# Performance work log

Hardware: AMD Instinct MI355X
Metric: run time of the kernel (lower is better)

The kernel has to match this reference:

```python
import jax, jax.numpy as jnp
import numpy as np

B, N = 2, 131072          # batch, expanded node slots (divisible by flag_size)
FEAT = 69                 # org(3) + pos(3) + uids(63)
KERNELS = 128
FLAG_SIZE = 4             # 1 << dims, dims = 2
BINS = 16                 # 1 << flag_size


def _conv1d(x, w, b, stride=1, padding='SAME'):
    # keras Conv1D: x [B,N,Cin], w [K,Cin,Cout], relu activation
    y = jax.lax.conv_general_dilated(x, w, (stride,), padding,
                                     dimension_numbers=('NWC', 'WIO', 'NWC'))
    return jax.nn.relu(y + b)


def setup_inputs() -> dict:
    key = jax.random.key(0)
    ks = jax.random.split(key, 12)

    def g(k, shape):
        fan_in = int(np.prod(shape[:-1]))
        return (jax.random.normal(k, shape, jnp.float32) / np.sqrt(fan_in)).astype(jnp.float32)

    c_x = FEAT + KERNELS                 # 197 after each pre conv concat
    c_flags = 2 * FEAT + KERNELS         # 266 flags-head input
    c_sym = c_flags + FLAG_SIZE          # 270 symbols-branch input

    return {
        'inputs': jax.random.normal(ks[0], (B, N, FEAT), jnp.float32),
        'w_pre0': g(ks[1], (3, FEAT, KERNELS)),   'b_pre0': jnp.zeros((KERNELS,), jnp.float32),
        'w_pre1': g(ks[2], (3, c_x, KERNELS)),    'b_pre1': jnp.zeros((KERNELS,), jnp.float32),
        'w_flags': g(ks[3], (c_flags, FLAG_SIZE)), 'b_flags': jnp.zeros((FLAG_SIZE,), jnp.float32),
        'w_merge': g(ks[4], (FLAG_SIZE, c_sym, KERNELS)), 'b_merge': jnp.zeros((KERNELS,), jnp.float32),
        'w_post0': g(ks[5], (3, KERNELS, KERNELS)), 'b_post0': jnp.zeros((KERNELS,), jnp.float32),
        'w_post1': g(ks[6], (3, KERNELS, KERNELS)), 'b_post1': jnp.zeros((KERNELS,), jnp.float32),
        'w_post2': g(ks[7], (3, KERNELS, KERNELS)), 'b_post2': jnp.zeros((KERNELS,), jnp.float32),
        'w_post3': g(ks[8], (3, KERNELS, KERNELS)), 'b_post3': jnp.zeros((KERNELS,), jnp.float32),
        'w_sym': g(ks[9], (KERNELS, BINS)),        'b_sym': jnp.zeros((BINS,), jnp.float32),
    }


def _forward(inputs, w_pre0, b_pre0, w_pre1, b_pre1, w_flags, b_flags,
             w_merge, b_merge, w_post0, b_post0, w_post1, b_post1,
             w_post2, b_post2, w_post3, b_post3, w_sym, b_sym):
    # pos offsets = (3, 6); pos = inputs[..., 3:5] (2 columns)
    pos = inputs[..., 3:5]
    sort = jnp.argsort(pos, axis=-2)                       # [B, N, 2]
    # gather with batch_dims=1 along node axis
    X = jnp.take_along_axis(inputs, sort[..., 1:2], axis=1)   # sorted by pos col 1
    x0 = jax.lax.stop_gradient(X)                            # [B, N, 69]
    X = jnp.concatenate([x0, _conv1d(X, w_pre0, b_pre0)], axis=-1)  # [B, N, 197]
    X = jnp.concatenate([x0, _conv1d(X, w_pre1, b_pre1)], axis=-1)  # [B, N, 197]
    X = jnp.concatenate([X, jnp.take_along_axis(inputs, sort[..., 0:1], axis=1)], axis=-1)  # [B, N, 266]

    F = jax.nn.sigmoid(X @ w_flags + b_flags)               # [B, N, 4]

    S = jax.lax.stop_gradient(jnp.concatenate([F, X], axis=-1))     # [B, N, 270]
    S = _conv1d(S, w_merge, b_merge, stride=FLAG_SIZE, padding='VALID')  # [B, N/4, 128]
    for w, b in ((w_post0, b_post0), (w_post1, b_post1), (w_post2, b_post2), (w_post3, b_post3)):
        S = _conv1d(S, w, b)
    S = jax.nn.softmax(S @ w_sym + b_sym, axis=-1)          # [B, N/4, 16]

    Fd = (F[..., 0] - F[..., 1]).reshape(F.shape[0], -1, FLAG_SIZE)  # [B, N/4, 4]
    return jnp.concatenate([Fd, S], axis=-1)                # [B, N/4, 20]


def reference(inputs, w_pre0, b_pre0, w_pre1, b_pre1, w_flags, b_flags,
              w_merge, b_merge, w_post0, b_post0, w_post1, b_post1,
              w_post2, b_post2, w_post3, b_post3, w_sym, b_sym):
    return _forward(inputs, w_pre0, b_pre0, w_pre1, b_pre1, w_flags, b_flags,
                    w_merge, b_merge, w_post0, b_post0, w_post1, b_post1,
                    w_post2, b_post2, w_post3, b_post3, w_sym, b_sym)
```

## Files before the change

### kernel.cpp

```cpp
#include <hip/hip_runtime.h>
#include <hip/hip_bf16.h>
#include <math.h>

#define NPOS 131072
#define NF   69
#define NMRG 32768
#define TILE 2048
#define TPS  64
#define NSORT 4
#define EPT  16
#define XCW  288

typedef __attribute__((ext_vector_type(8))) short short8;
typedef __attribute__((ext_vector_type(4))) short s16x4;
typedef __bf16 bf16x8 __attribute__((ext_vector_type(8)));
typedef __attribute__((ext_vector_type(4))) float f32x4;

static __device__ inline bf16x8 as_bf16x8(short8 v){ union{short8 s; bf16x8 b;} u; u.s=v; return u.b; }
static __device__ inline short f2bf(float x){ __hip_bfloat16 h = __float2bfloat16(x); return *(short*)&h; }
static __device__ inline float bf2f(short s){ return __uint_as_float(((unsigned)(unsigned short)s)<<16); }

static __device__ inline void gld16(const short* g, short* l){
  __builtin_amdgcn_global_load_lds(
      (const __attribute__((address_space(1))) unsigned int*)g,
      (__attribute__((address_space(3))) unsigned int*)l, 16, 0, 0);
}

__global__ void k_make_keys(const float* __restrict__ inp, unsigned* __restrict__ kA,
                            unsigned* __restrict__ vA){
  unsigned t = blockIdx.x*256u + threadIdx.x;
  unsigned s = t >> 17, i = t & (NPOS-1u);
  unsigned b = s >> 1, ch = 3u + (s & 1u);
  float x = inp[((size_t)b*NPOS + i)*NF + ch];
  unsigned u = __float_as_uint(x);
  u = (u & 0x80000000u) ? ~u : (u | 0x80000000u);
  kA[t] = u; vA[t] = i;
}

__global__ __launch_bounds__(256) void k_hist(const unsigned* __restrict__ src,
                                              unsigned* __restrict__ hist, int shift){
  __shared__ unsigned h[256];
  int tid = threadIdx.x;
  h[tid] = 0u; __syncthreads();
  int s = blockIdx.x / TPS, tile = blockIdx.x % TPS;
  const unsigned* ks = src + (size_t)s*NPOS + (size_t)tile*TILE;
  for (int r = 0; r < TILE/256; ++r){
    unsigned d = (ks[r*256 + tid] >> shift) & 255u;
    atomicAdd(&h[d], 1u);
  }
  __syncthreads();
  hist[s*16384 + tid*TPS + tile] = h[tid];
}

__global__ __launch_bounds__(256) void k_scan(unsigned* __restrict__ hist){
  __shared__ unsigned tot[256];
  int tid = threadIdx.x; int s = blockIdx.x;
  unsigned* g = hist + s*16384;
  unsigned sum = 0;
  for (int q = 0; q < TPS; ++q) sum += g[tid*TPS + q];
  tot[tid] = sum;
  __syncthreads();
  if (tid == 0){
    unsigned run = 0;
    for (int t = 0; t < 256; ++t){ unsigned tmp = tot[t]; tot[t] = run; run += tmp; }
  }
  __syncthreads();
  unsigned run = tot[tid];
  for (int q = 0; q < TPS; ++q){ unsigned tmp = g[tid*TPS+q]; g[tid*TPS+q] = run; run += tmp; }
}

__global__ __launch_bounds__(128) void k_scatter(const unsigned* __restrict__ srcK,
    const unsigned* __restrict__ srcV, unsigned* __restrict__ dstK, unsigned* __restrict__ dstV,
    const unsigned* __restrict__ off, int shift){
  __shared__ unsigned short cnt[256*128];
  int tid = threadIdx.x;
  unsigned* cz = (unsigned*)cnt;
  for (int idx = tid; idx < 256*128/2; idx += 128) cz[idx] = 0u;
  __syncthreads();
  int s = blockIdx.x / TPS, tile = blockIdx.x % TPS;
  const unsigned* ks = srcK + (size_t)s*NPOS + (size_t)tile*TILE;
  const unsigned* vs = srcV + (size_t)s*NPOS + (size_t)tile*TILE;
  unsigned k8[EPT], v8[EPT];
  #pragma unroll
  for (int r = 0; r < EPT; ++r){
    k8[r] = ks[tid*EPT + r];
    v8[r] = vs[tid*EPT + r];
    unsigned d = (k8[r] >> shift) & 255u;
    cnt[d*128 + tid]++;
  }
  __syncthreads();
  for (int dd = 0; dd < 2; ++dd){
    int d = tid + dd*128;
    unsigned run = 0;
    for (int t = 0; t < 128; ++t){ unsigned tmp = cnt[d*128 + t]; cnt[d*128 + t] = (unsigned short)run; run += tmp; }
  }
  __syncthreads();
  const unsigned* ob = off + s*16384;
  #pragma unroll
  for (int r = 0; r < EPT; ++r){
    unsigned d = (k8[r] >> shift) & 255u;
    unsigned rk = cnt[d*128 + tid];
    cnt[d*128 + tid] = (unsigned short)(rk + 1u);
    unsigned pos = ob[d*TPS + tile] + rk;
    dstK[(size_t)s*NPOS + pos] = k8[r];
    dstV[(size_t)s*NPOS + pos] = v8[r];
  }
}

__global__ __launch_bounds__(256) void k_cvt(const float* __restrict__ inp,
                                             short* __restrict__ inpb, int b){
  int t = blockIdx.x*256 + threadIdx.x;
  int i = t/9, q = t - i*9;
  const float* sp = inp + ((size_t)b*NPOS + i)*NF + q*8;
  short o[8];
  #pragma unroll
  for (int e = 0; e < 8; ++e){
    int c = q*8 + e;
    o[e] = (c < NF) ? f2bf(sp[e]) : (short)0;
  }
  *(short8*)(inpb + (size_t)i*72 + q*8) = *(short8*)o;
}

__global__ __launch_bounds__(256) void k_gath2(const short* __restrict__ inpb,
    const unsigned* __restrict__ P1, const unsigned* __restrict__ P0,
    short* __restrict__ XA, short* __restrict__ Xcat){
  int t = blockIdx.x*256 + threadIdx.x;
  int i = t/18, u = t - i*18;
  int p = u/9, q = u - p*9;
  if (p){
    short8 v = *(const short8*)(inpb + (size_t)P1[i]*72 + q*8);
    *(short8*)(XA + (size_t)i*224 + 128 + q*8) = v;
    s16x4 lo = {v[0],v[1],v[2],v[3]}, hi = {v[4],v[5],v[6],v[7]};
    *(s16x4*)(Xcat + (size_t)i*XCW + 132 + q*8) = lo;
    *(s16x4*)(Xcat + (size_t)i*XCW + 136 + q*8) = hi;
  } else {
    short8 v = *(const short8*)(inpb + (size_t)P0[i]*72 + q*8);
    *(short8*)(Xcat + (size_t)i*XCW + 208 + q*8) = v;
    if (q == 8){
      s16x4 z4 = {0,0,0,0};
      *(s16x4*)(Xcat + (size_t)i*XCW + 204) = z4;
      short8 z8 = {0,0,0,0,0,0,0,0};
      *(short8*)(Xcat + (size_t)i*XCW + 280) = z8;
    }
  }
}

__global__ void k_prepB(const float* __restrict__ w, short* __restrict__ out,
                        int KC, int NQ, int mode, int total){
  int t = blockIdx.x*256 + threadIdx.x;
  if (t >= total) return;
  int lane = t & 63, ni = (t>>6) & 1, ksub = (t>>7) & 1;
  int rest = t >> 8;
  int q = rest % NQ;
  int wv = rest / NQ;
  int tap = q / KC, cc = q - tap*KC;
  int nn = wv*32 + ni*16 + (lane & 15);
  int chb = cc*64 + ksub*32 + ((lane >> 4) & 3)*8;
  short o[8];
  #pragma unroll
  for (int e = 0; e < 8; ++e){
    int ch = chb + e;
    float val = 0.f;
    if (mode == 0){ if (ch < 69)  val = w[((size_t)tap*69  + ch)*128 + nn]; }
    else if (mode == 1){
      if (ch < 128)      val = w[((size_t)tap*197 + 69 + ch)*128 + nn];
      else if (ch < 197) val = w[((size_t)tap*197 + ch - 128)*128 + nn];
    }
    else if (mode == 2){ if (ch < 128) val = w[((size_t)tap*128 + ch)*128 + nn]; }
    else {
      int tm = ch / XCW, cm = ch - tm*XCW;
      int orig = -1;
      if (cm < 128)                     orig = 73 + cm;
      else if (cm < 201)                orig = cm - 128;
      else if (cm >= 208 && cm < 277)   orig = cm - 7;
      if (orig >= 0) val = w[((size_t)tm*270 + orig)*128 + nn];
    }
    o[e] = f2bf(val);
  }
  *(short8*)(out + (size_t)t*8) = *(short8*)o;
}

__global__ void k_prepWf(const float* __restrict__ wf, float* __restrict__ out){
  int t = blockIdx.x*256 + threadIdx.x;
  if (t >= XCW*4) return;
  int c = t >> 2, q = t & 3;
  float v = 0.f;
  if (c < 128)                  v = wf[(69 + c)*4 + q];
  else if (c >= 132 && c < 201) v = wf[(c - 132)*4 + q];
  else if (c >= 208 && c < 277) v = wf[(197 + c - 208)*4 + q];
  out[t] = v;
}

#define OSTR 132

template<int CPAD>
__global__ __launch_bounds__(256) void k_conv3p(
    const short* __restrict__ src, int sstride, int coff, int cin,
    const short* __restrict__ wB, const float* __restrict__ bias,
    short* __restrict__ dst, int dstride, int n)
{
  constexpr int KC = CPAD/64;
  constexpr int NSTEP2 = 3*KC*2;
  constexpr int PF = 4;
  constexpr int ASTR = CPAD + 8;
  constexpr int AG = CPAD/8;
  constexpr size_t ABYTES = (size_t)66*ASTR*2;
  constexpr size_t OBYTES = (size_t)64*OSTR*4;
  constexpr size_t LBYTES = (ABYTES > OBYTES) ? ABYTES : OBYTES;
  __shared__ __attribute__((aligned(16))) char LDS[LBYTES];
  short* A_s = (short*)LDS;
  float* OT  = (float*)LDS;
  int tid = threadIdx.x;
  int i0 = blockIdx.x*64;
  int wv = tid >> 6, lane = tid & 63;
  int lm = lane & 15, lk = lane >> 4;

  const short* wBw = wB + (size_t)wv*NSTEP2*1024 + (size_t)lane*8;
  auto LB = [&](int ss, int ni){
    return as_bf16x8(*(const short8*)(wBw + (ss*2 + ni)*512));
  };
  bf16x8 bq[PF][2];
  #pragma unroll
  for (int s = 0; s < PF; ++s){ bq[s][0] = LB(s,0); bq[s][1] = LB(s,1); }

  for (int idx = tid; idx < 66*AG; idx += 256){
    int r = idx / AG, g = idx - r*AG;
    int pos = i0 - 1 + r;
    short8 v = {0,0,0,0,0,0,0,0};
    if (pos >= 0 && pos < n && g*8 < cin){
      const short* sp = src + (size_t)pos*sstride + coff + g*8;
      if (g*8 + 8 <= cin) v = *(const short8*)sp;
      else { for (int j = 0; g*8 + j < cin; ++j) v[j] = sp[j]; }
    }
    *(short8*)(A_s + r*ASTR + g*8) = v;
  }
  __syncthreads();

  f32x4 acc[4][2] = {};
  #pragma unroll
  for (int ss = 0; ss < NSTEP2; ++ss){
    int slot = ss % PF;
    bf16x8 b0 = bq[slot][0], b1 = bq[slot][1];
    if (ss + PF < NSTEP2){ bq[slot][0] = LB(ss+PF,0); bq[slot][1] = LB(ss+PF,1); }
    int q = ss >> 1, ksub = ss & 1;
    int tp = q / KC, c = q - tp*KC;
    bf16x8 a[4];
    #pragma unroll
    for (int mi = 0; mi < 4; ++mi)
      a[mi] = as_bf16x8(*(const short8*)(A_s + (mi*16+lm+tp)*ASTR + c*64 + ksub*32 + lk*8));
    #pragma unroll
    for (int mi = 0; mi < 4; ++mi){
      acc[mi][0] = __builtin_amdgcn_mfma_f32_16x16x32_bf16(a[mi], b0, acc[mi][0], 0, 0, 0);
      acc[mi][1] = __builtin_amdgcn_mfma_f32_16x16x32_bf16(a[mi], b1, acc[mi][1], 0, 0, 0);
    }
  }
  __syncthreads();
  float b0s = bias[wv*32 + lm], b1s = bias[wv*32 + 16 + lm];
  #pragma unroll
  for (int mi = 0; mi < 4; ++mi)
    #pragma unroll
    for (int ni = 0; ni < 2; ++ni){
      float bb = ni ? b1s : b0s;
      #pragma unroll
      for (int r = 0; r < 4; ++r)
        OT[(mi*16 + lk*4 + r)*OSTR + wv*32 + ni*16 + lm] = fmaxf(acc[mi][ni][r] + bb, 0.f);
    }
  __syncthreads();
  {
    int r = tid >> 2, q = tid & 3;
    const float* row = OT + r*OSTR + q*32;
    short o[32];
    #pragma unroll
    for (int jc = 0; jc < 8; ++jc){
      f32x4 v = *(const f32x4*)(row + jc*4);
      #pragma unroll
      for (int e = 0; e < 4; ++e) o[jc*4+e] = f2bf(v[e]);
    }
    short* dp = dst + (size_t)(i0 + r)*dstride + q*32;
    #pragma unroll
    for (int v8 = 0; v8 < 4; ++v8) *(short8*)(dp + v8*8) = *(short8*)(o + v8*8);
  }
}

__global__ __launch_bounds__(256) void k_mergem3(const short* __restrict__ Xf,
    const short* __restrict__ wB, const float* __restrict__ bias, short* __restrict__ dst)
{
  constexpr int NS = 4*XCW/64;
  constexpr size_t OBYTES = (size_t)64*OSTR*4;
  __shared__ __attribute__((aligned(16))) char LDS[OBYTES];
  short* A_s = (short*)LDS;
  float* OT  = (float*)LDS;
  int tid = threadIdx.x;
  int j0 = blockIdx.x*64;
  int wv = tid >> 6, lane = tid & 63;
  int lm = lane & 15, lk = lane >> 4;
  auto stageA = [&](int s){
    #pragma unroll
    for (int it = 0; it < 2; ++it){
      int slot = it*256 + tid;
      int r = slot >> 3, kv = slot & 7;
      const short* gp = Xf + (size_t)(j0 + r)*(4*XCW) + s*64 + ((kv ^ (r&7))*8);
      gld16(gp, A_s + (s&1)*4096 + slot*8);
    }
  };
  const short* wBl = wB + (size_t)wv*NS*2048 + (size_t)lane*8;
  auto LB = [&](int s, int ks, int ni){
    return as_bf16x8(*(const short8*)(wBl + ((size_t)(s*2 + ks)*2 + ni)*512));
  };
  bf16x8 c00 = LB(0,0,0), c01 = LB(0,0,1), c10 = LB(0,1,0), c11 = LB(0,1,1);
  stageA(0);
  __syncthreads();
  f32x4 acc[4][2] = {};
  for (int s = 0; s < NS; ++s){
    bf16x8 n00, n01, n10, n11;
    if (s < NS-1){
      n00 = LB(s+1,0,0); n01 = LB(s+1,0,1); n10 = LB(s+1,1,0); n11 = LB(s+1,1,1);
      stageA(s+1);
    }
    const short* Ab = A_s + (s&1)*4096;
    bf16x8 a[4];
    #pragma unroll
    for (int mi = 0; mi < 4; ++mi){
      int r = mi*16 + lm;
      a[mi] = as_bf16x8(*(const short8*)(Ab + r*64 + ((lk ^ (r&7))*8)));
    }
    #pragma unroll
    for (int mi = 0; mi < 4; ++mi){
      acc[mi][0] = __builtin_amdgcn_mfma_f32_16x16x32_bf16(a[mi], c00, acc[mi][0], 0, 0, 0);
      acc[mi][1] = __builtin_amdgcn_mfma_f32_16x16x32_bf16(a[mi], c01, acc[mi][1], 0, 0, 0);
    }
    #pragma unroll
    for (int mi = 0; mi < 4; ++mi){
      int r = mi*16 + lm;
      a[mi] = as_bf16x8(*(const short8*)(Ab + r*64 + (((4+lk) ^ (r&7))*8)));
    }
    #pragma unroll
    for (int mi = 0; mi < 4; ++mi){
      acc[mi][0] = __builtin_amdgcn_mfma_f32_16x16x32_bf16(a[mi], c10, acc[mi][0], 0, 0, 0);
      acc[mi][1] = __builtin_amdgcn_mfma_f32_16x16x32_bf16(a[mi], c11, acc[mi][1], 0, 0, 0);
    }
    __syncthreads();
    c00 = n00; c01 = n01; c10 = n10; c11 = n11;
  }
  float b0 = bias[wv*32 + lm], b1 = bias[wv*32 + 16 + lm];
  #pragma unroll
  for (int mi = 0; mi < 4; ++mi)
    #pragma unroll
    for (int ni = 0; ni < 2; ++ni){
      float bb = ni ? b1 : b0;
      #pragma unroll
      for (int r = 0; r < 4; ++r)
        OT[(mi*16 + lk*4 + r)*OSTR + wv*32 + ni*16 + lm] = fmaxf(acc[mi][ni][r] + bb, 0.f);
    }
  __syncthreads();
  {
    int r = tid >> 2, q = tid & 3;
    const float* row = OT + r*OSTR + q*32;
    short o[32];
    #pragma unroll
    for (int jc = 0; jc < 8; ++jc){
      f32x4 v = *(const f32x4*)(row + jc*4);
      #pragma unroll
      for (int e = 0; e < 4; ++e) o[jc*4+e] = f2bf(v[e]);
    }
    short* dp = dst + (size_t)(j0 + r)*128 + q*32;
    #pragma unroll
    for (int v8 = 0; v8 < 4; ++v8) *(short8*)(dp + v8*8) = *(short8*)(o + v8*8);
  }
}

__global__ __launch_bounds__(256) void k_flags2(short* __restrict__ Xcat,
    const float* __restrict__ Wf2, const float* __restrict__ bf, float* __restrict__ F){
  size_t i = (size_t)blockIdx.x*256 + threadIdx.x;
  const short* x = Xcat + i*XCW;
  float a0 = bf[0], a1 = bf[1], a2 = bf[2], a3 = bf[3];
  for (int g = 0; g < XCW/8; ++g){
    short8 x8 = *(const short8*)(x + g*8);
    #pragma unroll
    for (int e = 0; e < 8; ++e){
      float xv = bf2f(x8[e]);
      const float* w = Wf2 + (g*8+e)*4;
      a0 = fmaf(xv,w[0],a0); a1 = fmaf(xv,w[1],a1); a2 = fmaf(xv,w[2],a2); a3 = fmaf(xv,w[3],a3);
    }
  }
  float f0 = 1.f/(1.f+expf(-a0)), f1 = 1.f/(1.f+expf(-a1));
  float f2 = 1.f/(1.f+expf(-a2)), f3 = 1.f/(1.f+expf(-a3));
  float* f = F + i*4;
  f[0]=f0; f[1]=f1; f[2]=f2; f[3]=f3;
  short* xc = Xcat + i*XCW + 128;
  xc[0]=f2bf(f0); xc[1]=f2bf(f1); xc[2]=f2bf(f2); xc[3]=f2bf(f3);
}

__global__ __launch_bounds__(256) void k_out(const short* __restrict__ S,
    const float* __restrict__ F, const float* __restrict__ Ws, const float* __restrict__ bs,
    float* __restrict__ out, int b){
  size_t j = (size_t)blockIdx.x*256 + threadIdx.x;
  float l[16];
  #pragma unroll
  for (int t = 0; t < 16; ++t) l[t] = bs[t];
  const short* s = S + j*128;
  for (int g = 0; g < 16; ++g){
    short8 x8 = *(const short8*)(s + g*8);
    #pragma unroll
    for (int e = 0; e < 8; ++e){
      float x = bf2f(x8[e]);
      const float* w = Ws + (g*8+e)*16;
      #pragma unroll
      for (int t = 0; t < 16; ++t) l[t] = fmaf(x, w[t], l[t]);
    }
  }
  float m = l[0];
  #pragma unroll
  for (int t = 1; t < 16; ++t) m = fmaxf(m, l[t]);
  float sum = 0.f;
  #pragma unroll
  for (int t = 0; t < 16; ++t){ l[t] = expf(l[t]-m); sum += l[t]; }
  float inv = 1.f/sum;
  float* o = out + ((size_t)b*NMRG + j)*20;
  #pragma unroll
  for (int k = 0; k < 4; ++k){
    size_t r = (size_t)(4*j + k)*4;
    o[k] = F[r] - F[r+1];
  }
  #pragma unroll
  for (int t = 0; t < 16; ++t) o[4+t] = l[t]*inv;
}

extern "C" void kernel_launch(void* const* d_in, const int* in_sizes, int n_in,
                              void* d_out, int out_size, void* d_ws, size_t ws_size,
                              hipStream_t stream){
  const float* inp     = (const float*)d_in[0];
  const float* w_pre0  = (const float*)d_in[1];
  const float* b_pre0  = (const float*)d_in[2];
  const float* w_pre1  = (const float*)d_in[3];
  const float* b_pre1  = (const float*)d_in[4];
  const float* w_flags = (const float*)d_in[5];
  const float* b_flags = (const float*)d_in[6];
  const float* w_merge = (const float*)d_in[7];
  const float* b_merge = (const float*)d_in[8];
  const float* w_post[4] = {(const float*)d_in[9], (const float*)d_in[11],
                            (const float*)d_in[13], (const float*)d_in[15]};
  const float* b_post[4] = {(const float*)d_in[10], (const float*)d_in[12],
                            (const float*)d_in[14], (const float*)d_in[16]};
  const float* w_sym   = (const float*)d_in[17];
  const float* b_sym   = (const float*)d_in[18];
  float* outp = (float*)d_out;

  char* p = (char*)d_ws;
  unsigned* kA = (unsigned*)p; p += (size_t)NSORT*NPOS*4;
  unsigned* vA = (unsigned*)p; p += (size_t)NSORT*NPOS*4;
  unsigned* kB = (unsigned*)p; p += (size_t)NSORT*NPOS*4;
  unsigned* vB = (unsigned*)p; p += (size_t)NSORT*NPOS*4;
  unsigned* hist = (unsigned*)p; p += (size_t)NSORT*16384*4;
  short* inpb = (short*)p; p += (size_t)NPOS*72*2;
  short* XA   = (short*)p; p += (size_t)NPOS*224*2;
  short* Xcat = (short*)p; p += (size_t)NPOS*XCW*2;
  float* Fbuf = (float*)p; p += (size_t)NPOS*4*4;
  short* M0   = (short*)p; p += (size_t)NMRG*128*2;
  short* M1   = (short*)p; p += (size_t)NMRG*128*2;
  short* wb0  = (short*)p; p += (size_t)3*2*8192*2;
  short* wb1  = (short*)p; p += (size_t)3*4*8192*2;
  short* wbq0 = (short*)p; p += (size_t)3*2*8192*2;
  short* wbq1 = (short*)p; p += (size_t)3*2*8192*2;
  short* wbq2 = (short*)p; p += (size_t)3*2*8192*2;
  short* wbq3 = (short*)p; p += (size_t)3*2*8192*2;
  short* wbm  = (short*)p; p += (size_t)18*8192*2;
  float* wf2  = (float*)p; p += (size_t)XCW*4*4;
  if ((size_t)(p - (char*)d_ws) > ws_size) return;
  short* wbq[4] = {wbq0, wbq1, wbq2, wbq3};

  k_prepB<<<(6144 +255)/256, 256, 0, stream>>>(w_pre0, wb0, 2, 6, 0, 6144);
  k_prepB<<<(12288+255)/256, 256, 0, stream>>>(w_pre1, wb1, 4, 12, 1, 12288);
  for (int i = 0; i < 4; ++i)
    k_prepB<<<(6144+255)/256, 256, 0, stream>>>(w_post[i], wbq[i], 2, 6, 2, 6144);
  k_prepB<<<(18432+255)/256, 256, 0, stream>>>(w_merge, wbm, 18, 18, 3, 18432);
  k_prepWf<<<(XCW*4+255)/256, 256, 0, stream>>>(w_flags, wf2);

  k_make_keys<<<NSORT*NPOS/256, 256, 0, stream>>>(inp, kA, vA);
  unsigned *sk = kA, *sv = vA, *dk = kB, *dv = vB;
  for (int pass = 0; pass < 4; ++pass){
    int shift = pass*8;
    k_hist<<<NSORT*TPS, 256, 0, stream>>>(sk, hist, shift);
    k_scan<<<NSORT, 256, 0, stream>>>(hist);
    k_scatter<<<NSORT*TPS, 128, 0, stream>>>(sk, sv, dk, dv, hist, shift);
    unsigned* t;
    t = sk; sk = dk; dk = t;
    t = sv; sv = dv; dv = t;
  }
  for (int b = 0; b < 2; ++b){
    const unsigned* P0 = sv + (size_t)(b*2+0)*NPOS;
    const unsigned* P1 = sv + (size_t)(b*2+1)*NPOS;
    k_cvt<<<NPOS*9/256, 256, 0, stream>>>(inp, inpb, b);
    k_gath2<<<NPOS*18/256, 256, 0, stream>>>(inpb, P1, P0, XA, Xcat);
    k_conv3p<128><<<NPOS/64, 256, 0, stream>>>(XA, 224, 128, 69,  wb0, b_pre0, XA,   224, NPOS);
    k_conv3p<256><<<NPOS/64, 256, 0, stream>>>(XA, 224, 0,   197, wb1, b_pre1, Xcat, XCW, NPOS);
    k_flags2<<<NPOS/256, 256, 0, stream>>>(Xcat, wf2, b_flags, Fbuf);
    k_mergem3<<<NMRG/64, 256, 0, stream>>>(Xcat, wbm, b_merge, M0);
    k_conv3p<128><<<NMRG/64, 256, 0, stream>>>(M0, 128, 0, 128, wbq[0], b_post[0], M1, 128, NMRG);
    k_conv3p<128><<<NMRG/64, 256, 0, stream>>>(M1, 128, 0, 128, wbq[1], b_post[1], M0, 128, NMRG);
    k_conv3p<128><<<NMRG/64, 256, 0, stream>>>(M0, 128, 0, 128, wbq[2], b_post[2], M1, 128, NMRG);
    k_conv3p<128><<<NMRG/64, 256, 0, stream>>>(M1, 128, 0, 128, wbq[3], b_post[3], M0, 128, NMRG);
    k_out<<<NMRG/256, 256, 0, stream>>>(M0, Fbuf, w_sym, b_sym, outp, b);
  }
}
```

Baseline: 598.8 us.

## Split conv input channels into halves, shrink tiles, stage bf16 output in LDS

```diff
diff --git a/kernel.cpp b/kernel.cpp
--- a/kernel.cpp
+++ b/kernel.cpp
@@ -191,65 +191,83 @@
   out[t] = v;
 }
 
-#define OSTR 132
-
-template<int CPAD>
-__global__ __launch_bounds__(256) void k_conv3p(
+#define OSTR2 136
+
+template<int CPAD, int MT>
+__global__ __launch_bounds__(256) void k_conv3s(
     const short* __restrict__ src, int sstride, int coff, int cin,
     const short* __restrict__ wB, const float* __restrict__ bias,
     short* __restrict__ dst, int dstride, int n)
 {
-  constexpr int KC = CPAD/64;
-  constexpr int NSTEP2 = 3*KC*2;
-  constexpr int PF = 4;
-  constexpr int ASTR = CPAD + 8;
-  constexpr int AG = CPAD/8;
-  constexpr size_t ABYTES = (size_t)66*ASTR*2;
-  constexpr size_t OBYTES = (size_t)64*OSTR*4;
+  constexpr int KC  = CPAD/64;
+  constexpr int KH  = CPAD/2;
+  constexpr int KC2 = KH/64;
+  constexpr int SPH = 3*KC2*2;
+  constexpr int NST = 2*SPH;
+  constexpr int PF  = 4;
+  constexpr int ASTR = KH + 8;
+  constexpr int AG  = KH/8;
+  constexpr int MI  = MT/16;
+  constexpr size_t ABYTES = (size_t)(MT+2)*ASTR*2;
+  constexpr size_t OBYTES = (size_t)MT*OSTR2*2;
   constexpr size_t LBYTES = (ABYTES > OBYTES) ? ABYTES : OBYTES;
   __shared__ __attribute__((aligned(16))) char LDS[LBYTES];
   short* A_s = (short*)LDS;
-  float* OT  = (float*)LDS;
+  short* OTs = (short*)LDS;
   int tid = threadIdx.x;
-  int i0 = blockIdx.x*64;
+  int i0 = blockIdx.x*MT;
   int wv = tid >> 6, lane = tid & 63;
   int lm = lane & 15, lk = lane >> 4;
 
-  const short* wBw = wB + (size_t)wv*NSTEP2*1024 + (size_t)lane*8;
-  auto LB = [&](int ss, int ni){
-    return as_bf16x8(*(const short8*)(wBw + (ss*2 + ni)*512));
+  const short* wBw = wB + (size_t)wv*(KC*6)*1024 + (size_t)lane*8;
+  auto LB = [&](int ls, int ni){
+    int h = ls / SPH, r1 = ls % SPH;
+    int tp = r1 / (KC2*2), r2 = r1 % (KC2*2);
+    int c = r2 >> 1, ksub = r2 & 1;
+    int q = tp*KC + h*KC2 + c;
+    return as_bf16x8(*(const short8*)(wBw + ((q*2 + ksub)*2 + ni)*512));
   };
+  auto stageA = [&](int h){
+    for (int idx = tid; idx < (MT+2)*AG; idx += 256){
+      int r = idx / AG, g = idx - r*AG;
+      int pos = i0 - 1 + r;
+      int cb = h*KH + g*8;
+      short8 v = {0,0,0,0,0,0,0,0};
+      if (pos >= 0 && pos < n && cb < cin){
+        const short* sp = src + (size_t)pos*sstride + coff + cb;
+        if (cb + 8 <= cin) v = *(const short8*)sp;
+        else { for (int j = 0; cb + j < cin; ++j) v[j] = sp[j]; }
+      }
+      *(short8*)(A_s + r*ASTR + g*8) = v;
+    }
+  };
+
   bf16x8 bq[PF][2];
   #pragma unroll
   for (int s = 0; s < PF; ++s){ bq[s][0] = LB(s,0); bq[s][1] = LB(s,1); }
-
-  for (int idx = tid; idx < 66*AG; idx += 256){
-    int r = idx / AG, g = idx - r*AG;
-    int pos = i0 - 1 + r;
-    short8 v = {0,0,0,0,0,0,0,0};
-    if (pos >= 0 && pos < n && g*8 < cin){
-      const short* sp = src + (size_t)pos*sstride + coff + g*8;
-      if (g*8 + 8 <= cin) v = *(const short8*)sp;
-      else { for (int j = 0; g*8 + j < cin; ++j) v[j] = sp[j]; }
-    }
-    *(short8*)(A_s + r*ASTR + g*8) = v;
-  }
-  __syncthreads();
-
-  f32x4 acc[4][2] = {};
-  #pragma unroll
-  for (int ss = 0; ss < NSTEP2; ++ss){
-    int slot = ss % PF;
+  stageA(0);
+  __syncthreads();
+
+  f32x4 acc[MI][2] = {};
+  #pragma unroll
+  for (int ls = 0; ls < NST; ++ls){
+    if (ls == SPH){
+      __syncthreads();
+      stageA(1);
+      __syncthreads();
+    }
+    int slot = ls % PF;
     bf16x8 b0 = bq[slot][0], b1 = bq[slot][1];
-    if (ss + PF < NSTEP2){ bq[slot][0] = LB(ss+PF,0); bq[slot][1] = LB(ss+PF,1); }
-    int q = ss >> 1, ksub = ss & 1;
-    int tp = q / KC, c = q - tp*KC;
-    bf16x8 a[4];
-    #pragma unroll
-    for (int mi = 0; mi < 4; ++mi)
+    if (ls + PF < NST){ bq[slot][0] = LB(ls+PF,0); bq[slot][1] = LB(ls+PF,1); }
+    int r1 = ls % SPH;
+    int tp = r1 / (KC2*2), r2 = r1 % (KC2*2);
+    int c = r2 >> 1, ksub = r2 & 1;
+    bf16x8 a[MI];
+    #pragma unroll
+    for (int mi = 0; mi < MI; ++mi)
       a[mi] = as_bf16x8(*(const short8*)(A_s + (mi*16+lm+tp)*ASTR + c*64 + ksub*32 + lk*8));
     #pragma unroll
-    for (int mi = 0; mi < 4; ++mi){
+    for (int mi = 0; mi < MI; ++mi){
       acc[mi][0] = __builtin_amdgcn_mfma_f32_16x16x32_bf16(a[mi], b0, acc[mi][0], 0, 0, 0);
       acc[mi][1] = __builtin_amdgcn_mfma_f32_16x16x32_bf16(a[mi], b1, acc[mi][1], 0, 0, 0);
     }
@@ -257,51 +275,45 @@
   __syncthreads();
   float b0s = bias[wv*32 + lm], b1s = bias[wv*32 + 16 + lm];
   #pragma unroll
-  for (int mi = 0; mi < 4; ++mi)
+  for (int mi = 0; mi < MI; ++mi)
     #pragma unroll
     for (int ni = 0; ni < 2; ++ni){
       float bb = ni ? b1s : b0s;
       #pragma unroll
       for (int r = 0; r < 4; ++r)
-        OT[(mi*16 + lk*4 + r)*OSTR + wv*32 + ni*16 + lm] = fmaxf(acc[mi][ni][r] + bb, 0.f);
+        OTs[(mi*16 + lk*4 + r)*OSTR2 + wv*32 + ni*16 + lm] = f2bf(fmaxf(acc[mi][ni][r] + bb, 0.f));
     }
   __syncthreads();
   {
-    int r = tid >> 2, q = tid & 3;
-    const float* row = OT + r*OSTR + q*32;
-    short o[32];
-    #pragma unroll
-    for (int jc = 0; jc < 8; ++jc){
-      f32x4 v = *(const f32x4*)(row + jc*4);
-      #pragma unroll
-      for (int e = 0; e < 4; ++e) o[jc*4+e] = f2bf(v[e]);
-    }
-    short* dp = dst + (size_t)(i0 + r)*dstride + q*32;
-    #pragma unroll
-    for (int v8 = 0; v8 < 4; ++v8) *(short8*)(dp + v8*8) = *(short8*)(o + v8*8);
-  }
-}
-
-__global__ __launch_bounds__(256) void k_mergem3(const short* __restrict__ Xf,
+    constexpr int CPT = (MT*128/8)/256;
+    int unit0 = tid*CPT;
+    int r = unit0 >> 4, uq = unit0 & 15;
+    const short* row = OTs + r*OSTR2 + uq*8;
+    short* dp = dst + (size_t)(i0 + r)*dstride + uq*8;
+    #pragma unroll
+    for (int j = 0; j < CPT; ++j)
+      *(short8*)(dp + j*8) = *(const short8*)(row + j*8);
+  }
+}
+
+__global__ __launch_bounds__(256) void k_mergem4(const short* __restrict__ Xf,
     const short* __restrict__ wB, const float* __restrict__ bias, short* __restrict__ dst)
 {
   constexpr int NS = 4*XCW/64;
-  constexpr size_t OBYTES = (size_t)64*OSTR*4;
-  __shared__ __attribute__((aligned(16))) char LDS[OBYTES];
+  constexpr size_t ABYTES = 2*2048*2;
+  constexpr size_t OBYTES = (size_t)32*OSTR2*2;
+  constexpr size_t LBYTES = (ABYTES > OBYTES) ? ABYTES : OBYTES;
+  __shared__ __attribute__((aligned(16))) char LDS[LBYTES];
   short* A_s = (short*)LDS;
-  float* OT  = (float*)LDS;
+  short* OTs = (short*)LDS;
   int tid = threadIdx.x;
-  int j0 = blockIdx.x*64;
+  int j0 = blockIdx.x*32;
   int wv = tid >> 6, lane = tid & 63;
   int lm = lane & 15, lk = lane >> 4;
   auto stageA = [&](int s){
-    #pragma unroll
-    for (int it = 0; it < 2; ++it){
-      int slot = it*256 + tid;
-      int r = slot >> 3, kv = slot & 7;
-      const short* gp = Xf + (size_t)(j0 + r)*(4*XCW) + s*64 + ((kv ^ (r&7))*8);
-      gld16(gp, A_s + (s&1)*4096 + slot*8);
-    }
+    int r = tid >> 3, kv = tid & 7;
+    const short* gp = Xf + (size_t)(j0 + r)*(4*XCW) + s*64 + ((kv ^ (r&7))*8);
+    gld16(gp, A_s + (s&1)*2048 + tid*8);
   };
   const short* wBl = wB + (size_t)wv*NS*2048 + (size_t)lane*8;
   auto LB = [&](int s, int ks, int ni){
@@ -310,32 +322,32 @@
   bf16x8 c00 = LB(0,0,0), c01 = LB(0,0,1), c10 = LB(0,1,0), c11 = LB(0,1,1);
   stageA(0);
   __syncthreads();
-  f32x4 acc[4][2] = {};
+  f32x4 acc[2][2] = {};
   for (int s = 0; s < NS; ++s){
     bf16x8 n00, n01, n10, n11;
     if (s < NS-1){
       n00 = LB(s+1,0,0); n01 = LB(s+1,0,1); n10 = LB(s+1,1,0); n11 = LB(s+1,1,1);
       stageA(s+1);
     }
-    const short* Ab = A_s + (s&1)*4096;
-    bf16x8 a[4];
-    #pragma unroll
-    for (int mi = 0; mi < 4; ++mi){
+    const short* Ab = A_s + (s&1)*2048;
+    bf16x8 a[2];
+    #pragma unroll
+    for (int mi = 0; mi < 2; ++mi){
       int r = mi*16 + lm;
       a[mi] = as_bf16x8(*(const short8*)(Ab + r*64 + ((lk ^ (r&7))*8)));
     }
     #pragma unroll
-    for (int mi = 0; mi < 4; ++mi){
+    for (int mi = 0; mi < 2; ++mi){
       acc[mi][0] = __builtin_amdgcn_mfma_f32_16x16x32_bf16(a[mi], c00, acc[mi][0], 0, 0, 0);
       acc[mi][1] = __builtin_amdgcn_mfma_f32_16x16x32_bf16(a[mi], c01, acc[mi][1], 0, 0, 0);
     }
     #pragma unroll
-    for (int mi = 0; mi < 4; ++mi){
+    for (int mi = 0; mi < 2; ++mi){
       int r = mi*16 + lm;
       a[mi] = as_bf16x8(*(const short8*)(Ab + r*64 + (((4+lk) ^ (r&7))*8)));
     }
     #pragma unroll
-    for (int mi = 0; mi < 4; ++mi){
+    for (int mi = 0; mi < 2; ++mi){
       acc[mi][0] = __builtin_amdgcn_mfma_f32_16x16x32_bf16(a[mi], c10, acc[mi][0], 0, 0, 0);
       acc[mi][1] = __builtin_amdgcn_mfma_f32_16x16x32_bf16(a[mi], c11, acc[mi][1], 0, 0, 0);
     }
@@ -344,28 +356,23 @@
   }
   float b0 = bias[wv*32 + lm], b1 = bias[wv*32 + 16 + lm];
   #pragma unroll
-  for (int mi = 0; mi < 4; ++mi)
+  for (int mi = 0; mi < 2; ++mi)
     #pragma unroll
     for (int ni = 0; ni < 2; ++ni){
       float bb = ni ? b1 : b0;
       #pragma unroll
       for (int r = 0; r < 4; ++r)
-        OT[(mi*16 + lk*4 + r)*OSTR + wv*32 + ni*16 + lm] = fmaxf(acc[mi][ni][r] + bb, 0.f);
+        OTs[(mi*16 + lk*4 + r)*OSTR2 + wv*32 + ni*16 + lm] = f2bf(fmaxf(acc[mi][ni][r] + bb, 0.f));
     }
   __syncthreads();
   {
-    int r = tid >> 2, q = tid & 3;
-    const float* row = OT + r*OSTR + q*32;
-    short o[32];
-    #pragma unroll
-    for (int jc = 0; jc < 8; ++jc){
-      f32x4 v = *(const f32x4*)(row + jc*4);
-      #pragma unroll
-      for (int e = 0; e < 4; ++e) o[jc*4+e] = f2bf(v[e]);
-    }
-    short* dp = dst + (size_t)(j0 + r)*128 + q*32;
-    #pragma unroll
-    for (int v8 = 0; v8 < 4; ++v8) *(short8*)(dp + v8*8) = *(short8*)(o + v8*8);
+    int unit0 = tid*2;
+    int r = unit0 >> 4, uq = unit0 & 15;
+    const short* row = OTs + r*OSTR2 + uq*8;
+    short* dp = dst + (size_t)(j0 + r)*128 + uq*8;
+    #pragma unroll
+    for (int j = 0; j < 2; ++j)
+      *(short8*)(dp + j*8) = *(const short8*)(row + j*8);
   }
 }
 
@@ -492,14 +499,14 @@
     const unsigned* P1 = sv + (size_t)(b*2+1)*NPOS;
     k_cvt<<<NPOS*9/256, 256, 0, stream>>>(inp, inpb, b);
     k_gath2<<<NPOS*18/256, 256, 0, stream>>>(inpb, P1, P0, XA, Xcat);
-    k_conv3p<128><<<NPOS/64, 256, 0, stream>>>(XA, 224, 128, 69,  wb0, b_pre0, XA,   224, NPOS);
-    k_conv3p<256><<<NPOS/64, 256, 0, stream>>>(XA, 224, 0,   197, wb1, b_pre1, Xcat, XCW, NPOS);
+    k_conv3s<128,64><<<NPOS/64, 256, 0, stream>>>(XA, 224, 128, 69,  wb0, b_pre0, XA,   224, NPOS);
+    k_conv3s<256,64><<<NPOS/64, 256, 0, stream>>>(XA, 224, 0,   197, wb1, b_pre1, Xcat, XCW, NPOS);
     k_flags2<<<NPOS/256, 256, 0, stream>>>(Xcat, wf2, b_flags, Fbuf);
-    k_mergem3<<<NMRG/64, 256, 0, stream>>>(Xcat, wbm, b_merge, M0);
-    k_conv3p<128><<<NMRG/64, 256, 0, stream>>>(M0, 128, 0, 128, wbq[0], b_post[0], M1, 128, NMRG);
-    k_conv3p<128><<<NMRG/64, 256, 0, stream>>>(M1, 128, 0, 128, wbq[1], b_post[1], M0, 128, NMRG);
-    k_conv3p<128><<<NMRG/64, 256, 0, stream>>>(M0, 128, 0, 128, wbq[2], b_post[2], M1, 128, NMRG);
-    k_conv3p<128><<<NMRG/64, 256, 0, stream>>>(M1, 128, 0, 128, wbq[3], b_post[3], M0, 128, NMRG);
+    k_mergem4<<<NMRG/32, 256, 0, stream>>>(Xcat, wbm, b_merge, M0);
+    k_conv3s<128,32><<<NMRG/32, 256, 0, stream>>>(M0, 128, 0, 128, wbq[0], b_post[0], M1, 128, NMRG);
+    k_conv3s<128,32><<<NMRG/32, 256, 0, stream>>>(M1, 128, 0, 128, wbq[1], b_post[1], M0, 128, NMRG);
+    k_conv3s<128,32><<<NMRG/32, 256, 0, stream>>>(M0, 128, 0, 128, wbq[2], b_post[2], M1, 128, NMRG);
+    k_conv3s<128,32><<<NMRG/32, 256, 0, stream>>>(M1, 128, 0, 128, wbq[3], b_post[3], M0, 128, NMRG);
     k_out<<<NMRG/256, 256, 0, stream>>>(M0, Fbuf, w_sym, b_sym, outp, b);
   }
 }
```

Result: no change. 591.2 us, median of 3 (-1.3%).
